# Performance work log

Measured on AMD Instinct MI355X. Metric: run time of the kernel, lower is better.

The kernel has to match this reference:

```python
import jax, jax.numpy as jnp
import numpy as np

B, S, D = 4, 2048, 1024
O = 1024
E = 8
K = 2

def setup_inputs() -> dict:
    key = jax.random.key(0)
    k1, k2, k3, k4, k5 = jax.random.split(key, 5)
    scale = 1.0 / np.sqrt(D)
    x = jax.random.normal(k1, (B, S, D), dtype=jnp.float32)
    # expert linear layers stacked: weight [E, D, O], bias [E, O]
    We = jax.random.uniform(k2, (E, D, O), dtype=jnp.float32, minval=-scale, maxval=scale)
    be = jax.random.uniform(k3, (E, O), dtype=jnp.float32, minval=-scale, maxval=scale)
    # gate linear: weight [D, E], bias [E]
    Wg = jax.random.uniform(k4, (D, E), dtype=jnp.float32, minval=-scale, maxval=scale)
    bg = jax.random.uniform(k5, (E,), dtype=jnp.float32, minval=-scale, maxval=scale)
    return {"x": x, "We": We, "be": be, "Wg": Wg, "bg": bg}

def reference(x, We, be, Wg, bg):
    b, s, d = x.shape
    x_flat = x.reshape(-1, d)                                   # [N, D]
    gates = jax.nn.softmax(x_flat @ Wg + bg, axis=-1)           # [N, E]
    topk_gates, topk_idx = jax.lax.top_k(gates, K)              # [N, K]
    topk_gates = topk_gates / jnp.sum(topk_gates, axis=1, keepdims=True)
    # dense all-expert compute (faithful to original naive MoE)
    expert_out = jnp.einsum('nd,edo->neo', x_flat, We) + be     # [N, E, O]
    # gather top-k expert outputs per token
    selected = jnp.take_along_axis(expert_out, topk_idx[:, :, None], axis=1)  # [N, K, O]
    out = jnp.sum(selected * topk_gates[:, :, None], axis=1)    # [N, O]
    return out.reshape(b, s, -1)
```

## Files before the change

kernel.cpp:

```cpp
#include <hip/hip_runtime.h>

#define N_TOK 8192
#define DDIM 1024
#define ODIM 1024
#define NEXP 8

typedef __attribute__((ext_vector_type(8))) short bf16x8;
typedef __attribute__((ext_vector_type(4))) float f32x4;

__device__ __forceinline__ unsigned int f2bf(float f) {
    unsigned int u = __float_as_uint(f);
    return (u + 0x7fffu + ((u >> 16) & 1u)) >> 16;
}
__device__ __forceinline__ float bflo(unsigned int u) { return __uint_as_float(u << 16); }
__device__ __forceinline__ float bfhi(unsigned int u) { return __uint_as_float(u & 0xffff0000u); }

__device__ __forceinline__ void async_copy16(const unsigned short* g, unsigned short* l) {
    __builtin_amdgcn_global_load_lds(
        (const __attribute__((address_space(1))) unsigned int*)g,
        (__attribute__((address_space(3))) unsigned int*)l, 16, 0, 0);
}

__global__ __launch_bounds__(256) void gate_kernel(const float* __restrict__ x,
                                                   const float* __restrict__ Wg,
                                                   const float* __restrict__ bg,
                                                   int* __restrict__ ea, int* __restrict__ eb,
                                                   float* __restrict__ ga, float* __restrict__ gb,
                                                   unsigned short* __restrict__ xbf,
                                                   int* __restrict__ counts) {
    if (blockIdx.x == 0) counts[threadIdx.x] = 0;
    const int wave = threadIdx.x >> 6, lane = threadIdx.x & 63;
    const int t = blockIdx.x * 4 + wave;
    const float* xr = x + (size_t)t * DDIM;

    float4 v[4];
#pragma unroll
    for (int c = 0; c < 4; ++c) v[c] = *(const float4*)&xr[c * 256 + lane * 4];

    unsigned short* xo = xbf + (size_t)t * DDIM;
#pragma unroll
    for (int c = 0; c < 4; ++c) {
        uint2 w;
        w.x = f2bf(v[c].x) | (f2bf(v[c].y) << 16);
        w.y = f2bf(v[c].z) | (f2bf(v[c].w) << 16);
        *(uint2*)&xo[c * 256 + lane * 4] = w;
    }

    float acc[8] = {0, 0, 0, 0, 0, 0, 0, 0};
#pragma unroll
    for (int c = 0; c < 4; ++c) {
        const int dbase = c * 256 + lane * 4;
#pragma unroll
        for (int j = 0; j < 4; ++j) {
            float xv = ((const float*)&v[c])[j];
            const float4* w = (const float4*)(Wg + (size_t)(dbase + j) * 8);
            float4 w0 = w[0], w1 = w[1];
            acc[0] += xv * w0.x; acc[1] += xv * w0.y; acc[2] += xv * w0.z; acc[3] += xv * w0.w;
            acc[4] += xv * w1.x; acc[5] += xv * w1.y; acc[6] += xv * w1.z; acc[7] += xv * w1.w;
        }
    }
#pragma unroll
    for (int off = 32; off > 0; off >>= 1) {
#pragma unroll
        for (int j = 0; j < 8; ++j) acc[j] += __shfl_xor(acc[j], off, 64);
    }
    if (lane == 0) {
        float s[8];
#pragma unroll
        for (int e = 0; e < 8; ++e) s[e] = acc[e] + bg[e];
        int a = 0;
#pragma unroll
        for (int e = 1; e < 8; ++e) if (s[e] > s[a]) a = e;
        int b = (a == 0) ? 1 : 0;
#pragma unroll
        for (int e = 0; e < 8; ++e) if (e != a && e != b && s[e] > s[b]) b = e;
        float g0 = 1.0f / (1.0f + __expf(s[b] - s[a]));
        ea[t] = a; eb[t] = b; ga[t] = g0; gb[t] = 1.0f - g0;
    }
}

__global__ __launch_bounds__(256) void transpose_kernel(const float* __restrict__ We,
                                                        unsigned short* __restrict__ WeT) {
    __shared__ float tile[64][65];
    const int lin = blockIdx.x;
    const int e = lin >> 8, rem = lin & 255;
    const int d0 = (rem >> 4) * 64, o0 = (rem & 15) * 64;
    const int tid = threadIdx.x;
#pragma unroll
    for (int p = 0; p < 4; ++p) {
        int idx = p * 256 + tid;
        int row = idx >> 4, c = idx & 15;
        float4 v = *(const float4*)&We[(((size_t)e * 1024 + d0 + row) << 10) + o0 + (c << 2)];
        tile[row][c * 4 + 0] = v.x; tile[row][c * 4 + 1] = v.y;
        tile[row][c * 4 + 2] = v.z; tile[row][c * 4 + 3] = v.w;
    }
    __syncthreads();
#pragma unroll
    for (int p = 0; p < 2; ++p) {
        int idx = p * 256 + tid;
        int orow = idx >> 3, c8 = idx & 7;
        unsigned int u[8];
#pragma unroll
        for (int j = 0; j < 8; ++j) u[j] = f2bf(tile[c8 * 8 + j][orow]);
        uint4 q;
        q.x = u[0] | (u[1] << 16); q.y = u[2] | (u[3] << 16);
        q.z = u[4] | (u[5] << 16); q.w = u[6] | (u[7] << 16);
        *(uint4*)&WeT[(((size_t)e * 1024 + o0 + orow) << 10) + d0 + (c8 << 3)] = q;
    }
}

__global__ __launch_bounds__(64) void scatter_kernel(const int* __restrict__ ea,
                                                     const int* __restrict__ eb,
                                                     int* __restrict__ counts,
                                                     int* __restrict__ btok,
                                                     int* __restrict__ slotA,
                                                     int* __restrict__ slotB) {
    const int t = blockIdx.x * 64 + threadIdx.x;
    const int lane = threadIdx.x & 63;
#pragma unroll
    for (int pass = 0; pass < 2; ++pass) {
        const int e = (pass == 0) ? ea[t] : eb[t];
        int* slot = (pass == 0) ? slotA : slotB;
#pragma unroll
        for (int ex = 0; ex < NEXP; ++ex) {
            unsigned long long mask = __ballot(e == ex);
            if (mask) {
                int leader = __ffsll((long long)mask) - 1;
                int base = 0;
                if (lane == leader) base = atomicAdd(&counts[ex * 32], __popcll(mask));
                base = __shfl(base, leader, 64);
                if (e == ex) {
                    int pos = base + __popcll(mask & ((1ull << lane) - 1ull));
                    btok[ex * N_TOK + pos] = t;
                    slot[t] = ex * N_TOK + pos;
                }
            }
        }
    }
}

__global__ __launch_bounds__(256, 2) void moe_gemm(const unsigned short* __restrict__ xbf,
                                                   const unsigned short* __restrict__ WeT,
                                                   const float* __restrict__ be,
                                                   const int* __restrict__ counts,
                                                   const int* __restrict__ btok,
                                                   unsigned short* __restrict__ ybuf) {
    const int id = blockIdx.x;
    const int e = id & 7;
    const int n0 = ((id >> 3) & 7) * 128;
    const int r0 = (id >> 6) * 128;
    const int cnt = counts[e * 32];
    if (r0 >= cnt) return;

    __shared__ unsigned short smem[32768];
    __shared__ int s_tok[128];

    const int tid = threadIdx.x;
    if (tid < 128) {
        int r = r0 + tid;
        int rc = (r < cnt) ? r : (cnt - 1);
        s_tok[tid] = btok[e * N_TOK + rc];
    }
    const int w = tid >> 6, lane = tid & 63;
    __syncthreads();

    const int rsub = lane >> 3;
    const int colo = ((lane & 7) ^ rsub) * 8;
    unsigned int a_off[4], b_off[4];
#pragma unroll
    for (int p = 0; p < 4; ++p) {
        int row = p * 32 + w * 8 + rsub;
        a_off[p] = ((unsigned)s_tok[row] << 10) + colo;
        b_off[p] = ((unsigned)(e * 1024 + n0 + row) << 10) + colo;
    }
    const int ldsrow = w * 8;

    const int wm = (w >> 1) * 64, wn = (w & 1) * 64;
    const int quad = lane >> 4, rA = lane & 15;
    const int sw = rA & 7;
    const int cs0 = (quad ^ sw) * 8;
    const int cs1 = ((4 + quad) ^ sw) * 8;

    f32x4 acc[4][4];
#pragma unroll
    for (int mi = 0; mi < 4; ++mi)
#pragma unroll
        for (int ni = 0; ni < 4; ++ni) acc[mi][ni] = (f32x4){0.f, 0.f, 0.f, 0.f};

#pragma unroll
    for (int p = 0; p < 4; ++p) {
        async_copy16(xbf + a_off[p], &smem[(p * 32 + ldsrow) * 64]);
        async_copy16(WeT + b_off[p], &smem[16384 + (p * 32 + ldsrow) * 64]);
    }
#pragma unroll
    for (int p = 0; p < 4; ++p) {
        async_copy16(xbf + a_off[p] + 64, &smem[8192 + (p * 32 + ldsrow) * 64]);
        async_copy16(WeT + b_off[p] + 64, &smem[24576 + (p * 32 + ldsrow) * 64]);
    }
    asm volatile("s_waitcnt vmcnt(8)" ::: "memory");
    __builtin_amdgcn_s_barrier();
    __builtin_amdgcn_sched_barrier(0);

    bf16x8 a0[4], b0[4];
#pragma unroll
    for (int i = 0; i < 4; ++i) {
        a0[i] = *(bf16x8*)&smem[(wm + i * 16 + rA) * 64 + cs0];
        b0[i] = *(bf16x8*)&smem[16384 + (wn + i * 16 + rA) * 64 + cs0];
    }

    for (int t = 0; t < 16; ++t) {
        const int cur = t & 1;
        unsigned short* sAc = smem + cur * 8192;
        unsigned short* sBc = smem + 16384 + cur * 8192;
        unsigned short* sAn = smem + (cur ^ 1) * 8192;
        unsigned short* sBn = smem + 16384 + (cur ^ 1) * 8192;

        bf16x8 a1[4], b1[4];
#pragma unroll
        for (int i = 0; i < 4; ++i) {
            a1[i] = *(bf16x8*)&sAc[(wm + i * 16 + rA) * 64 + cs1];
            b1[i] = *(bf16x8*)&sBc[(wn + i * 16 + rA) * 64 + cs1];
        }
        __builtin_amdgcn_s_setprio(1);
#pragma unroll
        for (int mi = 0; mi < 4; ++mi)
#pragma unroll
            for (int ni = 0; ni < 4; ++ni)
                acc[mi][ni] = __builtin_amdgcn_mfma_f32_16x16x32_bf16(b0[ni], a0[mi], acc[mi][ni], 0, 0, 0);
        __builtin_amdgcn_s_setprio(0);

        asm volatile("s_waitcnt lgkmcnt(0)" ::: "memory");
        __builtin_amdgcn_sched_barrier(0);
        __builtin_amdgcn_s_barrier();
        __builtin_amdgcn_sched_barrier(0);

        if (t < 14) {
            const int ko = (t + 2) * 64;
#pragma unroll
            for (int p = 0; p < 4; ++p) {
                async_copy16(xbf + a_off[p] + ko, &sAc[(p * 32 + ldsrow) * 64]);
                async_copy16(WeT + b_off[p] + ko, &sBc[(p * 32 + ldsrow) * 64]);
            }
        }
        if (t < 15) {
            if (t < 14) {
                asm volatile("s_waitcnt vmcnt(8)" ::: "memory");
            } else {
                asm volatile("s_waitcnt vmcnt(0)" ::: "memory");
            }
            __builtin_amdgcn_sched_barrier(0);
            __builtin_amdgcn_s_barrier();
            __builtin_amdgcn_sched_barrier(0);
#pragma unroll
            for (int i = 0; i < 4; ++i) {
                a0[i] = *(bf16x8*)&sAn[(wm + i * 16 + rA) * 64 + cs0];
                b0[i] = *(bf16x8*)&sBn[(wn + i * 16 + rA) * 64 + cs0];
            }
        }

        __builtin_amdgcn_s_setprio(1);
#pragma unroll
        for (int mi = 0; mi < 4; ++mi)
#pragma unroll
            for (int ni = 0; ni < 4; ++ni)
                acc[mi][ni] = __builtin_amdgcn_mfma_f32_16x16x32_bf16(b1[ni], a1[mi], acc[mi][ni], 0, 0, 0);
        __builtin_amdgcn_s_setprio(0);
    }

    float4 bv[4];
#pragma unroll
    for (int ni = 0; ni < 4; ++ni)
        bv[ni] = *(const float4*)&be[(e << 10) + n0 + wn + ni * 16 + quad * 4];
#pragma unroll
    for (int mi = 0; mi < 4; ++mi) {
        const int lrow = wm + mi * 16 + rA;
        if (r0 + lrow < cnt) {
            unsigned short* yrow =
                ybuf + (((size_t)(e * N_TOK + r0 + lrow)) << 10) + n0 + wn + quad * 4;
#pragma unroll
            for (int ni = 0; ni < 4; ++ni) {
                uint2 pk;
                pk.x = f2bf(acc[mi][ni][0] + bv[ni].x) | (f2bf(acc[mi][ni][1] + bv[ni].y) << 16);
                pk.y = f2bf(acc[mi][ni][2] + bv[ni].z) | (f2bf(acc[mi][ni][3] + bv[ni].w) << 16);
                *(uint2*)&yrow[ni * 16] = pk;
            }
        }
    }
}

__global__ __launch_bounds__(256) void combine_kernel(const unsigned short* __restrict__ ybuf,
                                                      const int* __restrict__ slotA,
                                                      const int* __restrict__ slotB,
                                                      const float* __restrict__ ga,
                                                      const float* __restrict__ gb,
                                                      float* __restrict__ out) {
    const int wave = threadIdx.x >> 6, lane = threadIdx.x & 63;
    const int t = blockIdx.x * 4 + wave;
    const unsigned short* ra = ybuf + ((size_t)slotA[t] << 10);
    const unsigned short* rb = ybuf + ((size_t)slotB[t] << 10);
    const float a = ga[t], b = gb[t];
    float* orow = out + ((size_t)t << 10);
#pragma unroll
    for (int i = 0; i < 2; ++i) {
        int c = i * 512 + lane * 8;
        uint4 ua = *(const uint4*)&ra[c];
        uint4 ub = *(const uint4*)&rb[c];
        float4 o0, o1;
        o0.x = a * bflo(ua.x) + b * bflo(ub.x);
        o0.y = a * bfhi(ua.x) + b * bfhi(ub.x);
        o0.z = a * bflo(ua.y) + b * bflo(ub.y);
        o0.w = a * bfhi(ua.y) + b * bfhi(ub.y);
        o1.x = a * bflo(ua.z) + b * bflo(ub.z);
        o1.y = a * bfhi(ua.z) + b * bfhi(ub.z);
        o1.z = a * bflo(ua.w) + b * bflo(ub.w);
        o1.w = a * bfhi(ua.w) + b * bfhi(ub.w);
        *(float4*)&orow[c] = o0;
        *(float4*)&orow[c + 4] = o1;
    }
}

extern "C" void kernel_launch(void* const* d_in, const int* in_sizes, int n_in,
                              void* d_out, int out_size, void* d_ws, size_t ws_size,
                              hipStream_t stream) {
    const float* x  = (const float*)d_in[0];
    const float* We = (const float*)d_in[1];
    const float* be = (const float*)d_in[2];
    const float* Wg = (const float*)d_in[3];
    const float* bg = (const float*)d_in[4];
    float* out = (float*)d_out;

    char* ws = (char*)d_ws;
    size_t off = 0;
    int* counts = (int*)(ws + off); off += 8 * 32 * 4;
    int* btok   = (int*)(ws + off); off += NEXP * N_TOK * 4;
    int* slotA  = (int*)(ws + off); off += N_TOK * 4;
    int* slotB  = (int*)(ws + off); off += N_TOK * 4;
    int* ea = (int*)(ws + off); off += N_TOK * 4;
    int* eb = (int*)(ws + off); off += N_TOK * 4;
    float* ga = (float*)(ws + off); off += N_TOK * 4;
    float* gb = (float*)(ws + off); off += N_TOK * 4;
    unsigned short* WeT  = (unsigned short*)(ws + off); off += (size_t)NEXP * DDIM * ODIM * 2;
    unsigned short* xbf  = (unsigned short*)(ws + off); off += (size_t)N_TOK * DDIM * 2;
    unsigned short* ybuf = (unsigned short*)(ws + off); off += (size_t)NEXP * N_TOK * ODIM * 2;

    gate_kernel<<<dim3(2048), 256, 0, stream>>>(x, Wg, bg, ea, eb, ga, gb, xbf, counts);
    transpose_kernel<<<dim3(2048), 256, 0, stream>>>(We, WeT);
    scatter_kernel<<<dim3(N_TOK / 64), 64, 0, stream>>>(ea, eb, counts, btok, slotA, slotB);
    moe_gemm<<<dim3(64 * 8 * 8), 256, 0, stream>>>(xbf, WeT, be, counts, btok, ybuf);
    combine_kernel<<<dim3(N_TOK / 4), 256, 0, stream>>>(ybuf, slotA, slotB, ga, gb, out);
}
```

Baseline: 217.8 us.

## Widen MoE GEMM tile to 128x256 with 8 waves and ping-pong quadrant schedule

The grouped expert GEMM now uses 512-thread blocks that each compute a 128x256 output tile instead of 128x128, halving the number of blocks and the re-reading of gathered token rows. The K loop is split into four MFMA quadrants, with the async global-to-LDS loads for the next stages interleaved between them and separated by barriers. This is meant to improve reuse of A tiles and overlap memory with compute. In exchange it uses more LDS (96KB B+A double buffer), more barriers per iteration, and fewer blocks for load balance across experts.

After: 234.7 us. 7.8% more time.

```diff
diff --git a/kernel.cpp b/kernel.cpp
--- a/kernel.cpp
+++ b/kernel.cpp
@@ -139,7 +139,7 @@
     }
 }
 
-__global__ __launch_bounds__(256, 2) void moe_gemm(const unsigned short* __restrict__ xbf,
+__global__ __launch_bounds__(512, 2) void moe_gemm(const unsigned short* __restrict__ xbf,
                                                    const unsigned short* __restrict__ WeT,
                                                    const float* __restrict__ be,
                                                    const int* __restrict__ counts,
@@ -147,12 +147,12 @@
                                                    unsigned short* __restrict__ ybuf) {
     const int id = blockIdx.x;
     const int e = id & 7;
-    const int n0 = ((id >> 3) & 7) * 128;
-    const int r0 = (id >> 6) * 128;
+    const int n0 = ((id >> 3) & 3) * 256;
+    const int r0 = (id >> 5) * 128;
     const int cnt = counts[e * 32];
     if (r0 >= cnt) return;
 
-    __shared__ unsigned short smem[32768];
+    __shared__ unsigned short smem[49152];
     __shared__ int s_tok[128];
 
     const int tid = threadIdx.x;
@@ -162,20 +162,28 @@
         s_tok[tid] = btok[e * N_TOK + rc];
     }
     const int w = tid >> 6, lane = tid & 63;
+    const int wr = w >> 2, wc = w & 3;
     __syncthreads();
 
     const int rsub = lane >> 3;
     const int colo = ((lane & 7) ^ rsub) * 8;
-    unsigned int a_off[4], b_off[4];
-#pragma unroll
-    for (int p = 0; p < 4; ++p) {
-        int row = p * 32 + w * 8 + rsub;
-        a_off[p] = ((unsigned)s_tok[row] << 10) + colo;
-        b_off[p] = ((unsigned)(e * 1024 + n0 + row) << 10) + colo;
-    }
-    const int ldsrow = w * 8;
-
-    const int wm = (w >> 1) * 64, wn = (w & 1) * 64;
+    unsigned int a_off[2];
+#pragma unroll
+    for (int p = 0; p < 2; ++p)
+        a_off[p] = ((unsigned)s_tok[p * 64 + w * 8 + rsub] << 10) + colo;
+    const int a_row0[2] = {0 * 64 + w * 8, 1 * 64 + w * 8};
+    unsigned int b_off[2][2];
+    int b_row0[2][2];
+#pragma unroll
+    for (int nh = 0; nh < 2; ++nh)
+#pragma unroll
+        for (int p = 0; p < 2; ++p) {
+            int c = (p * 2 + wr) * 64 + nh * 32 + wc * 8;
+            b_row0[nh][p] = c;
+            b_off[nh][p] = ((unsigned)(e * 1024 + n0 + c + rsub) << 10) + colo;
+        }
+
+    const int wm = wr * 64, wn = wc * 64;
     const int quad = lane >> 4, rA = lane & 15;
     const int sw = rA & 7;
     const int cs0 = (quad ^ sw) * 8;
@@ -188,83 +196,131 @@
         for (int ni = 0; ni < 4; ++ni) acc[mi][ni] = (f32x4){0.f, 0.f, 0.f, 0.f};
 
 #pragma unroll
-    for (int p = 0; p < 4; ++p) {
-        async_copy16(xbf + a_off[p], &smem[(p * 32 + ldsrow) * 64]);
-        async_copy16(WeT + b_off[p], &smem[16384 + (p * 32 + ldsrow) * 64]);
-    }
-#pragma unroll
-    for (int p = 0; p < 4; ++p) {
-        async_copy16(xbf + a_off[p] + 64, &smem[8192 + (p * 32 + ldsrow) * 64]);
-        async_copy16(WeT + b_off[p] + 64, &smem[24576 + (p * 32 + ldsrow) * 64]);
-    }
-    asm volatile("s_waitcnt vmcnt(8)" ::: "memory");
+    for (int p = 0; p < 2; ++p)
+        async_copy16(xbf + a_off[p], &smem[a_row0[p] * 64]);
+#pragma unroll
+    for (int nh = 0; nh < 2; ++nh)
+#pragma unroll
+        for (int p = 0; p < 2; ++p)
+            async_copy16(WeT + b_off[nh][p], &smem[16384 + b_row0[nh][p] * 64]);
+#pragma unroll
+    for (int p = 0; p < 2; ++p)
+        async_copy16(xbf + a_off[p] + 64, &smem[8192 + a_row0[p] * 64]);
+#pragma unroll
+    for (int p = 0; p < 2; ++p)
+        async_copy16(WeT + b_off[0][p] + 64, &smem[32768 + b_row0[0][p] * 64]);
+    asm volatile("s_waitcnt vmcnt(4)" ::: "memory");
     __builtin_amdgcn_s_barrier();
     __builtin_amdgcn_sched_barrier(0);
 
-    bf16x8 a0[4], b0[4];
-#pragma unroll
-    for (int i = 0; i < 4; ++i) {
-        a0[i] = *(bf16x8*)&smem[(wm + i * 16 + rA) * 64 + cs0];
-        b0[i] = *(bf16x8*)&smem[16384 + (wn + i * 16 + rA) * 64 + cs0];
-    }
+    bf16x8 af[4][2], bf[4][2];
 
     for (int t = 0; t < 16; ++t) {
         const int cur = t & 1;
         unsigned short* sAc = smem + cur * 8192;
-        unsigned short* sBc = smem + 16384 + cur * 8192;
-        unsigned short* sAn = smem + (cur ^ 1) * 8192;
-        unsigned short* sBn = smem + 16384 + (cur ^ 1) * 8192;
-
-        bf16x8 a1[4], b1[4];
-#pragma unroll
-        for (int i = 0; i < 4; ++i) {
-            a1[i] = *(bf16x8*)&sAc[(wm + i * 16 + rA) * 64 + cs1];
-            b1[i] = *(bf16x8*)&sBc[(wn + i * 16 + rA) * 64 + cs1];
-        }
+        unsigned short* sBc = smem + 16384 + cur * 16384;
+        unsigned short* sBn = smem + 16384 + (cur ^ 1) * 16384;
+
+#pragma unroll
+        for (int mi = 0; mi < 2; ++mi) {
+            af[mi][0] = *(bf16x8*)&sAc[(wm + mi * 16 + rA) * 64 + cs0];
+            af[mi][1] = *(bf16x8*)&sAc[(wm + mi * 16 + rA) * 64 + cs1];
+        }
+#pragma unroll
+        for (int ni = 0; ni < 2; ++ni) {
+            bf[ni][0] = *(bf16x8*)&sBc[(wn + ni * 16 + rA) * 64 + cs0];
+            bf[ni][1] = *(bf16x8*)&sBc[(wn + ni * 16 + rA) * 64 + cs1];
+        }
+        if (t < 15) {
+            const int ko = (t + 1) * 64;
+#pragma unroll
+            for (int p = 0; p < 2; ++p)
+                async_copy16(WeT + b_off[1][p] + ko, &sBn[b_row0[1][p] * 64]);
+        }
+        __builtin_amdgcn_s_barrier();
+        asm volatile("s_waitcnt lgkmcnt(0)" ::: "memory");
+        __builtin_amdgcn_sched_barrier(0);
         __builtin_amdgcn_s_setprio(1);
 #pragma unroll
-        for (int mi = 0; mi < 4; ++mi)
-#pragma unroll
-            for (int ni = 0; ni < 4; ++ni)
-                acc[mi][ni] = __builtin_amdgcn_mfma_f32_16x16x32_bf16(b0[ni], a0[mi], acc[mi][ni], 0, 0, 0);
+        for (int mi = 0; mi < 2; ++mi)
+#pragma unroll
+            for (int ni = 0; ni < 2; ++ni) {
+                acc[mi][ni] = __builtin_amdgcn_mfma_f32_16x16x32_bf16(bf[ni][0], af[mi][0], acc[mi][ni], 0, 0, 0);
+                acc[mi][ni] = __builtin_amdgcn_mfma_f32_16x16x32_bf16(bf[ni][1], af[mi][1], acc[mi][ni], 0, 0, 0);
+            }
         __builtin_amdgcn_s_setprio(0);
-
-        asm volatile("s_waitcnt lgkmcnt(0)" ::: "memory");
-        __builtin_amdgcn_sched_barrier(0);
-        __builtin_amdgcn_s_barrier();
-        __builtin_amdgcn_sched_barrier(0);
-
+        __builtin_amdgcn_s_barrier();
+        __builtin_amdgcn_sched_barrier(0);
+
+#pragma unroll
+        for (int mi = 2; mi < 4; ++mi) {
+            af[mi][0] = *(bf16x8*)&sAc[(wm + mi * 16 + rA) * 64 + cs0];
+            af[mi][1] = *(bf16x8*)&sAc[(wm + mi * 16 + rA) * 64 + cs1];
+        }
         if (t < 14) {
             const int ko = (t + 2) * 64;
 #pragma unroll
-            for (int p = 0; p < 4; ++p) {
-                async_copy16(xbf + a_off[p] + ko, &sAc[(p * 32 + ldsrow) * 64]);
-                async_copy16(WeT + b_off[p] + ko, &sBc[(p * 32 + ldsrow) * 64]);
-            }
-        }
-        if (t < 15) {
-            if (t < 14) {
-                asm volatile("s_waitcnt vmcnt(8)" ::: "memory");
-            } else {
-                asm volatile("s_waitcnt vmcnt(0)" ::: "memory");
-            }
-            __builtin_amdgcn_sched_barrier(0);
-            __builtin_amdgcn_s_barrier();
-            __builtin_amdgcn_sched_barrier(0);
-#pragma unroll
-            for (int i = 0; i < 4; ++i) {
-                a0[i] = *(bf16x8*)&sAn[(wm + i * 16 + rA) * 64 + cs0];
-                b0[i] = *(bf16x8*)&sBn[(wn + i * 16 + rA) * 64 + cs0];
-            }
-        }
-
+            for (int p = 0; p < 2; ++p)
+                async_copy16(WeT + b_off[0][p] + ko, &sBc[b_row0[0][p] * 64]);
+        }
+        __builtin_amdgcn_s_barrier();
+        asm volatile("s_waitcnt lgkmcnt(0)" ::: "memory");
+        __builtin_amdgcn_sched_barrier(0);
         __builtin_amdgcn_s_setprio(1);
 #pragma unroll
-        for (int mi = 0; mi < 4; ++mi)
-#pragma unroll
-            for (int ni = 0; ni < 4; ++ni)
-                acc[mi][ni] = __builtin_amdgcn_mfma_f32_16x16x32_bf16(b1[ni], a1[mi], acc[mi][ni], 0, 0, 0);
+        for (int mi = 2; mi < 4; ++mi)
+#pragma unroll
+            for (int ni = 0; ni < 2; ++ni) {
+                acc[mi][ni] = __builtin_amdgcn_mfma_f32_16x16x32_bf16(bf[ni][0], af[mi][0], acc[mi][ni], 0, 0, 0);
+                acc[mi][ni] = __builtin_amdgcn_mfma_f32_16x16x32_bf16(bf[ni][1], af[mi][1], acc[mi][ni], 0, 0, 0);
+            }
         __builtin_amdgcn_s_setprio(0);
+        __builtin_amdgcn_s_barrier();
+        __builtin_amdgcn_sched_barrier(0);
+
+#pragma unroll
+        for (int ni = 2; ni < 4; ++ni) {
+            bf[ni][0] = *(bf16x8*)&sBc[(wn + ni * 16 + rA) * 64 + cs0];
+            bf[ni][1] = *(bf16x8*)&sBc[(wn + ni * 16 + rA) * 64 + cs1];
+        }
+        if (t < 14) {
+            const int ko = (t + 2) * 64;
+#pragma unroll
+            for (int p = 0; p < 2; ++p)
+                async_copy16(xbf + a_off[p] + ko, &sAc[a_row0[p] * 64]);
+        }
+        __builtin_amdgcn_s_barrier();
+        asm volatile("s_waitcnt lgkmcnt(0)" ::: "memory");
+        __builtin_amdgcn_sched_barrier(0);
+        __builtin_amdgcn_s_setprio(1);
+#pragma unroll
+        for (int mi = 0; mi < 2; ++mi)
+#pragma unroll
+            for (int ni = 2; ni < 4; ++ni) {
+                acc[mi][ni] = __builtin_amdgcn_mfma_f32_16x16x32_bf16(bf[ni][0], af[mi][0], acc[mi][ni], 0, 0, 0);
+                acc[mi][ni] = __builtin_amdgcn_mfma_f32_16x16x32_bf16(bf[ni][1], af[mi][1], acc[mi][ni], 0, 0, 0);
+            }
+        __builtin_amdgcn_s_setprio(0);
+        __builtin_amdgcn_s_barrier();
+        __builtin_amdgcn_sched_barrier(0);
+
+        __builtin_amdgcn_s_setprio(1);
+#pragma unroll
+        for (int mi = 2; mi < 4; ++mi)
+#pragma unroll
+            for (int ni = 2; ni < 4; ++ni) {
+                acc[mi][ni] = __builtin_amdgcn_mfma_f32_16x16x32_bf16(bf[ni][0], af[mi][0], acc[mi][ni], 0, 0, 0);
+                acc[mi][ni] = __builtin_amdgcn_mfma_f32_16x16x32_bf16(bf[ni][1], af[mi][1], acc[mi][ni], 0, 0, 0);
+            }
+        __builtin_amdgcn_s_setprio(0);
+        if (t < 14) {
+            asm volatile("s_waitcnt vmcnt(4)" ::: "memory");
+        } else if (t == 14) {
+            asm volatile("s_waitcnt vmcnt(0)" ::: "memory");
+        }
+        __builtin_amdgcn_sched_barrier(0);
+        __builtin_amdgcn_s_barrier();
+        __builtin_amdgcn_sched_barrier(0);
     }
 
     float4 bv[4];
@@ -346,6 +402,6 @@
     gate_kernel<<<dim3(2048), 256, 0, stream>>>(x, Wg, bg, ea, eb, ga, gb, xbf, counts);
     transpose_kernel<<<dim3(2048), 256, 0, stream>>>(We, WeT);
     scatter_kernel<<<dim3(N_TOK / 64), 64, 0, stream>>>(ea, eb, counts, btok, slotA, slotB);
-    moe_gemm<<<dim3(64 * 8 * 8), 256, 0, stream>>>(xbf, WeT, be, counts, btok, ybuf);
+    moe_gemm<<<dim3(64 * 4 * 8), 512, 0, stream>>>(xbf, WeT, be, counts, btok, ybuf);
     combine_kernel<<<dim3(N_TOK / 4), 256, 0, stream>>>(ybuf, slotA, slotB, ga, gb, out);
 }
```
